# Optimization experiments

Hardware: AMD Instinct MI355X
Metric: run time of the kernel (lower is better)

The kernel has to match this reference:

```python
import jax, jax.numpy as jnp
import numpy as np

N = 131072        # total nodes
D = 256           # d_model (params.emb_dim)
STEPS = 16        # depth steps
G = N // STEPS    # nodes per depth step (equal-sized groups)
B = 16            # batch (number of trees); all lengths equal N//B
V = 1024          # len(id2word)
# op schedule: -1 leaf embedding, -2 numeric encoder, 0/1 unary ('sin','cos'), 2/3 binary ('add','mul')
SCHEDULE = [-1, -2, 0, 2, 1, 3, 0, 2, 1, 3, 0, 2, 1, 3, 0, 2]


def setup_inputs() -> dict:
    key = jax.random.key(0)
    ks = jax.random.split(key, 8)
    tokens = jax.random.randint(ks[0], (N,), 0, V, dtype=jnp.int32)
    # children of a node at depth d must already be computed: indices < d*G
    rng = np.random.default_rng(0)
    li = np.zeros(N, np.int32)
    ri = np.zeros(N, np.int32)
    for d in range(2, STEPS):
        li[d * G:(d + 1) * G] = rng.integers(0, d * G, G)
        ri[d * G:(d + 1) * G] = rng.integers(0, d * G, G)
    depths = jnp.repeat(jnp.arange(STEPS, dtype=jnp.int32), G)
    operation_order = jnp.array(SCHEDULE, dtype=jnp.int32)
    lengths = jnp.full((B,), N // B, dtype=jnp.int32)
    s = 0.05
    leaf_table = jax.random.normal(ks[1], (V, D), jnp.float32)
    num_W1 = jax.random.normal(ks[2], (D, 1), jnp.float32) * s
    num_b1 = jnp.zeros((D,), jnp.float32)
    num_W2 = jax.random.normal(ks[3], (D, D), jnp.float32) * s
    num_b2 = jnp.zeros((D,), jnp.float32)
    una_W = jax.random.normal(ks[4], (2, 4, D, D), jnp.float32) * s
    una_b = jnp.zeros((2, 4, D), jnp.float32)
    bin_W = jax.random.normal(ks[5], (2, 10, D, D), jnp.float32) * s
    bin_b = jnp.zeros((2, 5, D), jnp.float32)
    return dict(tokens=tokens, left_idx=jnp.asarray(li), right_idx=jnp.asarray(ri),
                depths=depths, operation_order=operation_order, lengths=lengths,
                leaf_table=leaf_table, num_W1=num_W1, num_b1=num_b1,
                num_W2=num_W2, num_b2=num_b2,
                una_W=una_W, una_b=una_b, bin_W=bin_W, bin_b=bin_b)


def _unary_cell(hc, W, b):
    # hc: [G, 2, D]; W: [4, D, D] (data, forget, output, input); b: [4, D]
    h, c = hc[:, 0], hc[:, 1]
    g = jnp.einsum('nd,ked->kne', h, W) + b[:, None, :]  # y = h @ W_k.T + b_k
    i = jax.nn.sigmoid(g[0])
    f = jax.nn.sigmoid(g[1])
    o = jax.nn.sigmoid(g[2])
    u = jnp.tanh(g[3])
    c2 = i * u + f * c
    h2 = o * jnp.tanh(c2)
    h2 = h2 / jnp.linalg.norm(h2)  # global (Frobenius) norm, as in torch h.norm(p=2)
    c2 = c2 / jnp.linalg.norm(c2)
    return jnp.stack([h2, c2], axis=1)


def _binary_cell(hcl, hcr, W, b):
    # W: [10, D, D] = (data_l, data_r, f_ll, f_lr, f_rl, f_rr, out_l, out_r, in_l, in_r)
    # b: [5, D] = (data, forget_l, forget_r, output, input)
    hl, cl = hcl[:, 0], hcl[:, 1]
    hr, cr = hcr[:, 0], hcr[:, 1]
    gl = jnp.einsum('nd,ked->kne', hl, W[jnp.array([0, 2, 4, 6, 8])])
    gr = jnp.einsum('nd,ked->kne', hr, W[jnp.array([1, 3, 5, 7, 9])])
    g = gl + gr + b[:, None, :]
    i = jax.nn.sigmoid(g[0])
    f_l = jax.nn.sigmoid(g[1])
    f_r = jax.nn.sigmoid(g[2])
    o = jax.nn.sigmoid(g[3])
    u = jnp.tanh(g[4])
    c2 = i * u + f_l * cl + f_r * cr
    h2 = o * jnp.tanh(c2)
    h2 = h2 / jnp.linalg.norm(h2)
    c2 = c2 / jnp.linalg.norm(c2)
    return jnp.stack([h2, c2], axis=1)


def reference(tokens, left_idx, right_idx, depths, operation_order, lengths,
              leaf_table, num_W1, num_b1, num_W2, num_b2,
              una_W, una_b, bin_W, bin_b):
    sched = np.asarray(operation_order).tolist()  # static dispatch schedule
    n = tokens.shape[0]
    steps = len(sched)
    g = n // steps
    d_model = leaf_table.shape[1]
    acts = jnp.zeros((n, 2, d_model), leaf_table.dtype)
    for d, op in enumerate(sched):
        s = d * g
        if op == -1:  # leaf embedding with max_norm=1.0 renorm (non-differentiable scale)
            e = leaf_table[tokens[s:s + g]]
            nrm = jnp.linalg.norm(e, axis=-1, keepdims=True)
            scale = jax.lax.stop_gradient(jnp.minimum(1.0, 1.0 / (nrm + 1e-7)))
            e = e * scale
            step_act = jnp.stack([e, jnp.zeros_like(e)], axis=1)
        elif op == -2:  # numeric encoder
            x = tokens[s:s + g].astype(leaf_table.dtype)[:, None]
            h1 = jax.nn.sigmoid(x @ num_W1.T + num_b1)
            e = jax.nn.sigmoid(h1 @ num_W2.T + num_b2)
            step_act = jnp.stack([e, jnp.zeros_like(e)], axis=1)
        elif op in (0, 1):  # unary LSTM cell: gather child then cell
            child = acts[left_idx[s:s + g]]
            step_act = _unary_cell(child, una_W[op], una_b[op])
        else:  # binary LSTM cell: gather both children
            l = acts[left_idx[s:s + g]]
            r = acts[right_idx[s:s + g]]
            step_act = _binary_cell(l, r, bin_W[op - 2], bin_b[op - 2])
        acts = jax.lax.dynamic_update_slice(acts, step_act, (s, 0, 0))
    hidden = acts[:, 0, :]  # [N, D]
    batch = lengths.shape[0]
    # all lengths equal -> pad_sequence is a reshape: [B, L, D]
    return hidden.reshape(batch, n // batch, d_model)
```

## Files before the change

### kernel.cpp

```cpp
#include <hip/hip_runtime.h>
#include <hip/hip_bf16.h>
#include <cstdint>

typedef unsigned short u16;
typedef unsigned int u32;
typedef __attribute__((ext_vector_type(4))) float floatx4;
typedef __attribute__((ext_vector_type(8))) short shortx8;

#define G_STEP 8192
#define N_TOTAL 131072
#define RHALF (1280*256)

__device__ __forceinline__ float bfu2f(u16 x){ return __uint_as_float(((unsigned)x)<<16); }
__device__ __forceinline__ u16 f2bfu(float x){ __hip_bfloat16 b = __float2bfloat16(x); return *reinterpret_cast<u16*>(&b); }
__device__ __forceinline__ float sigm(float x){ return 1.0f/(1.0f+__expf(-x)); }
__device__ __forceinline__ float tanh_(float x){
  float cx = fminf(fmaxf(x,-15.f),15.f);
  float e = __expf(2.f*cx);
  return (e-1.f)/(e+1.f);
}
__device__ __forceinline__ float invs(float x){ return 1.0f/sqrtf(x); }

__device__ __forceinline__ void gl16(const void* g, void* l){
  __builtin_amdgcn_global_load_lds((const __attribute__((address_space(1))) u32*)g,
                                   (__attribute__((address_space(3))) u32*)l, 16, 0, 0);
}

template<int V> __device__ __forceinline__ void wait_vml();
template<> __device__ __forceinline__ void wait_vml<0>(){ asm volatile("s_waitcnt vmcnt(0) lgkmcnt(0)" ::: "memory"); }
template<> __device__ __forceinline__ void wait_vml<6>(){ asm volatile("s_waitcnt vmcnt(6) lgkmcnt(0)" ::: "memory"); }
template<> __device__ __forceinline__ void wait_vml<7>(){ asm volatile("s_waitcnt vmcnt(7) lgkmcnt(0)" ::: "memory"); }

__device__ __forceinline__ void cvt8(const float* __restrict__ src, u16* __restrict__ dst){
  float4 a = *reinterpret_cast<const float4*>(src);
  float4 b = *reinterpret_cast<const float4*>(src+4);
  ushort4 o0; o0.x=f2bfu(a.x); o0.y=f2bfu(a.y); o0.z=f2bfu(a.z); o0.w=f2bfu(a.w);
  ushort4 o1; o1.x=f2bfu(b.x); o1.y=f2bfu(b.y); o1.z=f2bfu(b.z); o1.w=f2bfu(b.w);
  *reinterpret_cast<ushort4*>(dst)   = o0;
  *reinterpret_cast<ushort4*>(dst+4) = o1;
}

__global__ __launch_bounds__(256) void setup_kernel(
    const int* __restrict__ tokens, const float* __restrict__ leaf_table,
    const float* __restrict__ W1, const float* __restrict__ b1,
    const float* __restrict__ una_W, const float* __restrict__ bin_W,
    const float* __restrict__ num_W2,
    u16* __restrict__ wbu, u16* __restrict__ wbb, u16* __restrict__ wbn,
    u16* __restrict__ h1, u16* __restrict__ H, u16* __restrict__ C,
    float* __restrict__ sumsq)
{
  const int b = blockIdx.x, tid = threadIdx.x;
  if (b < 256){
    int row = b*8 + (tid>>5), d0 = (tid&31)*8;
    int op = row>>10, w = row&1023;
    int gate = (w>>4)&3, e = ((w>>6)<<4) | (w&15);
    cvt8(una_W + (size_t)((op*4+gate)*256 + e)*256 + d0, wbu + (size_t)row*256 + d0);
  } else if (b < 896){
    int row = (b-256)*8 + (tid>>5), d0 = (tid&31)*8;
    int ob = row / 2560, rem = row - ob*2560;
    int lr = rem / 1280, rw = rem - lr*1280;
    int eblk = rw / 80, rem2 = rw - eblk*80;
    int gate = rem2 >> 4, el = rem2 & 15;
    int e = eblk*16 + el;
    cvt8(bin_W + (size_t)((ob*10 + 2*gate + lr)*256 + e)*256 + d0, wbb + (size_t)row*256 + d0);
  } else if (b < 928){
    int row = (b-896)*8 + (tid>>5), d0 = (tid&31)*8;
    cvt8(num_W2 + (size_t)row*256 + d0, wbn + (size_t)row*256 + d0);
  } else if (b < 2976){
    int wave = tid >> 6, lane = tid & 63;
    int node = (b-928)*4 + wave;
    int t = tokens[node];
    const float4 e4 = *reinterpret_cast<const float4*>(leaf_table + (size_t)t*256 + lane*4);
    float ss = e4.x*e4.x + e4.y*e4.y + e4.z*e4.z + e4.w*e4.w;
    #pragma unroll
    for (int o = 32; o; o >>= 1) ss += __shfl_down(ss, o);
    ss = __shfl(ss, 0);
    float scale = fminf(1.0f, 1.0f/(sqrtf(ss) + 1e-7f));
    ushort4 hv;
    hv.x = f2bfu(e4.x*scale); hv.y = f2bfu(e4.y*scale);
    hv.z = f2bfu(e4.z*scale); hv.w = f2bfu(e4.w*scale);
    ushort4 zv; zv.x = zv.y = zv.z = zv.w = 0;
    *reinterpret_cast<ushort4*>(H + (size_t)node*256 + lane*4) = hv;
    *reinterpret_cast<ushort4*>(C + (size_t)node*256 + lane*4) = zv;
  } else if (b < 4000){
    int flat = (b-2976)*2048 + tid*8;
    int n = flat >> 8, d0 = flat & 255;
    float x = (float)tokens[G_STEP + n];
    float4 w0 = *reinterpret_cast<const float4*>(W1 + d0);
    float4 w1 = *reinterpret_cast<const float4*>(W1 + d0 + 4);
    float4 c0 = *reinterpret_cast<const float4*>(b1 + d0);
    float4 c1 = *reinterpret_cast<const float4*>(b1 + d0 + 4);
    ushort4 o0, o1;
    o0.x = f2bfu(sigm(x*w0.x + c0.x)); o0.y = f2bfu(sigm(x*w0.y + c0.y));
    o0.z = f2bfu(sigm(x*w0.z + c0.z)); o0.w = f2bfu(sigm(x*w0.w + c0.w));
    o1.x = f2bfu(sigm(x*w1.x + c1.x)); o1.y = f2bfu(sigm(x*w1.y + c1.y));
    o1.z = f2bfu(sigm(x*w1.z + c1.z)); o1.w = f2bfu(sigm(x*w1.w + c1.w));
    *reinterpret_cast<ushort4*>(h1 + flat)     = o0;
    *reinterpret_cast<ushort4*>(h1 + flat + 4) = o1;
  } else {
    if (tid < 32) sumsq[tid] = ((tid & 15) < 2) ? 1.0f : 0.0f;
  }
}

template<int MODE>
__global__ __launch_bounds__(512, 2) void gemm_fused(
    const u16* __restrict__ Asrc, const int* __restrict__ lidx,
    const int* __restrict__ ridx, const u16* __restrict__ Wb,
    const float* __restrict__ bias, const u16* __restrict__ Cin,
    float* __restrict__ sumsq, u16* __restrict__ H, u16* __restrict__ C,
    int sbase, int step)
{
  constexpr int NG  = (MODE==0) ? 1 : (MODE==1 ? 4 : 5);
  constexpr int NBR = (MODE==2) ? 160 : 128;
  constexpr int NT  = (MODE==2) ? 8 : 4;
  constexpr int WN  = (MODE==2) ? 80 : 64;
  constexpr int NFR = WN/16;
  constexpr int NBG = NBR/8;

  __shared__ u16 SA[3][256][64];
  __shared__ u16 SB[3][NBR][64];
  __shared__ float scH[16];
  __shared__ float scC[16];
  __shared__ float red[16];

  const int tid  = threadIdx.x;
  const int lane = tid & 63, wave = tid >> 6;

  const int bid = blockIdx.x;
  const int jj  = bid >> 3;
  const int bx  = (bid & 7) + 8*(jj & 3);
  const int by  = jj >> 2;
  const int mbase = bx*256;
  const int nbase = by*NBR;

  const int l15 = lane & 15, kg = lane >> 4;
  const int wm = (wave >> 1)*64, wn = (wave & 1)*WN;

  if (MODE != 0){
    if (tid < 16)      scH[tid]    = invs(sumsq[tid]);
    else if (tid < 32) scC[tid-16] = invs(sumsq[tid]);
  }

  const int rhi = lane >> 3;
  const int lc  = (lane & 7) ^ rhi;

  const u16* aL[4]; const u16* aR[4];
  #pragma unroll
  for (int g = 0; g < 4; g++){
    int r = (wave*4 + g)*8 + rhi;
    int gr;
    if constexpr (MODE==0) gr = mbase + r;
    else                   gr = lidx[sbase + mbase + r];
    aL[g] = Asrc + (size_t)gr*256 + lc*8;
    if constexpr (MODE==2)
      aR[g] = Asrc + (size_t)ridx[sbase + mbase + r]*256 + lc*8;
  }
  const int nbg_w = (MODE==2) ? ((wave < 4) ? 3 : 2) : 2;
  const int bg0   = (MODE==2) ? ((wave < 4) ? wave*3 : 12 + (wave-4)*2) : wave*2;
  const u16* bP[3];
  #pragma unroll
  for (int g = 0; g < 3; g++){
    int gg = bg0 + g;
    if (gg >= NBG) gg = NBG-1;
    bP[g] = Wb + (size_t)(nbase + gg*8 + rhi)*256 + lc*8;
  }

  floatx4 accL[4][NFR];
  #pragma unroll
  for (int i = 0; i < 4; i++)
    #pragma unroll
    for (int j2 = 0; j2 < NFR; j2++) accL[i][j2] = (floatx4)(0.0f);
  floatx4 accR[(MODE==2)?4:1][(MODE==2)?NFR:1];
  if constexpr (MODE==2){
    #pragma unroll
    for (int i = 0; i < 4; i++)
      #pragma unroll
      for (int j2 = 0; j2 < NFR; j2++) accR[i][j2] = (floatx4)(0.0f);
  }

  auto stage = [&](int t){
    const int slot = t % 3;
    const int kk = t*64;
    #pragma unroll
    for (int g = 0; g < 4; g++){
      const u16* ga;
      if constexpr (MODE==2){ ga = (kk >= 256) ? aR[g] + (kk-256) : aL[g] + kk; }
      else                  { ga = aL[g] + kk; }
      gl16(ga, &SA[slot][(wave*4 + g)*8][0]);
    }
    #pragma unroll
    for (int g = 0; g < 3; g++){
      if (g < nbg_w){
        const u16* gb;
        if constexpr (MODE==2){ gb = (kk >= 256) ? bP[g] + RHALF + (kk-256) : bP[g] + kk; }
        else                  { gb = bP[g] + kk; }
        gl16(gb, &SB[slot][(bg0 + g)*8][0]);
      }
    }
  };

  stage(0);
  stage(1);
  if (MODE==2 && wave < 4) wait_vml<7>(); else wait_vml<6>();
  __builtin_amdgcn_s_barrier();

  #pragma unroll
  for (int t = 0; t < NT; t++){
    const int slot = t % 3;
    if (t + 2 < NT) stage(t+2);

    {
      shortx8 af[4], bfr[NFR];
      const int pc = (kg ^ (l15 & 7)) * 8;
      #pragma unroll
      for (int i = 0; i < 4; i++)
        af[i] = *reinterpret_cast<const shortx8*>(&SA[slot][wm + i*16 + l15][pc]);
      #pragma unroll
      for (int n = 0; n < NFR; n++)
        bfr[n] = *reinterpret_cast<const shortx8*>(&SB[slot][wn + n*16 + l15][pc]);
      if (MODE==2 && t >= 4){
        #pragma unroll
        for (int mi = 0; mi < 4; mi++)
          #pragma unroll
          for (int ni = 0; ni < NFR; ni++)
            accR[mi][ni] = __builtin_amdgcn_mfma_f32_16x16x32_bf16(af[mi], bfr[ni], accR[mi][ni], 0, 0, 0);
      } else {
        #pragma unroll
        for (int mi = 0; mi < 4; mi++)
          #pragma unroll
          for (int ni = 0; ni < NFR; ni++)
            accL[mi][ni] = __builtin_amdgcn_mfma_f32_16x16x32_bf16(af[mi], bfr[ni], accL[mi][ni], 0, 0, 0);
      }
    }
    {
      shortx8 af[4], bfr[NFR];
      const int pc = ((4 + kg) ^ (l15 & 7)) * 8;
      #pragma unroll
      for (int i = 0; i < 4; i++)
        af[i] = *reinterpret_cast<const shortx8*>(&SA[slot][wm + i*16 + l15][pc]);
      #pragma unroll
      for (int n = 0; n < NFR; n++)
        bfr[n] = *reinterpret_cast<const shortx8*>(&SB[slot][wn + n*16 + l15][pc]);
      if (MODE==2 && t >= 4){
        #pragma unroll
        for (int mi = 0; mi < 4; mi++)
          #pragma unroll
          for (int ni = 0; ni < NFR; ni++)
            accR[mi][ni] = __builtin_amdgcn_mfma_f32_16x16x32_bf16(af[mi], bfr[ni], accR[mi][ni], 0, 0, 0);
      } else {
        #pragma unroll
        for (int mi = 0; mi < 4; mi++)
          #pragma unroll
          for (int ni = 0; ni < NFR; ni++)
            accL[mi][ni] = __builtin_amdgcn_mfma_f32_16x16x32_bf16(af[mi], bfr[ni], accL[mi][ni], 0, 0, 0);
      }
    }

    if (t + 1 < NT){
      if (t + 2 < NT){
        if (MODE==2 && wave < 4) wait_vml<7>(); else wait_vml<6>();
      } else wait_vml<0>();
      __builtin_amdgcn_s_barrier();
    }
  }

  if constexpr (MODE == 0){
    float bb[4];
    #pragma unroll
    for (int ni = 0; ni < 4; ni++) bb[ni] = bias[nbase + wn + ni*16 + l15];
    #pragma unroll
    for (int mi = 0; mi < 4; mi++){
      #pragma unroll
      for (int r = 0; r < 4; r++){
        int node = sbase + mbase + wm + mi*16 + kg*4 + r;
        u16* hp = H + (size_t)node*256 + nbase + wn + l15;
        u16* cp = C + (size_t)node*256 + nbase + wn + l15;
        #pragma unroll
        for (int ni = 0; ni < 4; ni++){
          hp[ni*16] = f2bfu(sigm(accL[mi][ni][r] + bb[ni]));
          cp[ni*16] = 0;
        }
      }
    }
  } else {
    const int eb = by*2 + (wave & 1);
    const int e  = eb*16 + l15;
    float bb[NG];
    #pragma unroll
    for (int g = 0; g < NG; g++) bb[g] = bias[g*256 + e];
    float hss = 0.f, css = 0.f;
    #pragma unroll
    for (int mi = 0; mi < 4; mi++){
      #pragma unroll
      for (int r = 0; r < 4; r++){
        int orow = mbase + wm + mi*16 + kg*4 + r;
        int node = sbase + orow;
        int chl = lidx[node];
        float sl = scH[chl >> 13];
        float cl = bfu2f(Cin[(size_t)chl*256 + e]) * scC[chl >> 13];
        float c2, h2;
        if constexpr (MODE == 1){
          float i_ = sigm(accL[mi][0][r]*sl + bb[0]);
          float f_ = sigm(accL[mi][1][r]*sl + bb[1]);
          float o_ = sigm(accL[mi][2][r]*sl + bb[2]);
          float u_ = tanh_(accL[mi][3][r]*sl + bb[3]);
          c2 = i_*u_ + f_*cl;
          h2 = o_*tanh_(c2);
        } else {
          int chr = ridx[node];
          float sr = scH[chr >> 13];
          float cr = bfu2f(Cin[(size_t)chr*256 + e]) * scC[chr >> 13];
          float g0 = accL[mi][0][r]*sl + accR[mi][0][r]*sr + bb[0];
          float g1 = accL[mi][1][r]*sl + accR[mi][1][r]*sr + bb[1];
          float g2 = accL[mi][2][r]*sl + accR[mi][2][r]*sr + bb[2];
          float g3 = accL[mi][3][r]*sl + accR[mi][3][r]*sr + bb[3];
          float g4 = accL[mi][4][r]*sl + accR[mi][4][r]*sr + bb[4];
          float i_ = sigm(g0);
          float fl = sigm(g1);
          float fr = sigm(g2);
          float o_ = sigm(g3);
          float u_ = tanh_(g4);
          c2 = i_*u_ + fl*cl + fr*cr;
          h2 = o_*tanh_(c2);
        }
        H[(size_t)node*256 + e] = f2bfu(h2);
        C[(size_t)node*256 + e] = f2bfu(c2);
        hss += h2*h2;
        css += c2*c2;
      }
    }
    #pragma unroll
    for (int o = 32; o; o >>= 1){ hss += __shfl_down(hss, o); css += __shfl_down(css, o); }
    if (lane == 0){ red[wave] = hss; red[8+wave] = css; }
    __syncthreads();
    if (tid == 0){
      float s = 0.f;
      #pragma unroll
      for (int w = 0; w < 8; w++) s += red[w];
      atomicAdd(&sumsq[step], s);
    }
    if (tid == 64){
      float s = 0.f;
      #pragma unroll
      for (int w = 0; w < 8; w++) s += red[8+w];
      atomicAdd(&sumsq[16 + step], s);
    }
  }
}

__global__ __launch_bounds__(256) void out_kernel(
    const u16* __restrict__ H, const float* __restrict__ sumsq, float* __restrict__ out)
{
  size_t base = ((size_t)blockIdx.x*256 + threadIdx.x)*8;
  int n = (int)(base >> 8);
  float s = invs(sumsq[n >> 13]);
  const uint4 v = *reinterpret_cast<const uint4*>(H + base);
  float4 o0, o1;
  o0.x = bfu2f((u16)(v.x & 0xffff))*s; o0.y = bfu2f((u16)(v.x >> 16))*s;
  o0.z = bfu2f((u16)(v.y & 0xffff))*s; o0.w = bfu2f((u16)(v.y >> 16))*s;
  o1.x = bfu2f((u16)(v.z & 0xffff))*s; o1.y = bfu2f((u16)(v.z >> 16))*s;
  o1.z = bfu2f((u16)(v.w & 0xffff))*s; o1.w = bfu2f((u16)(v.w >> 16))*s;
  *reinterpret_cast<float4*>(out + base)     = o0;
  *reinterpret_cast<float4*>(out + base + 4) = o1;
}

extern "C" void kernel_launch(void* const* d_in, const int* in_sizes, int n_in,
                              void* d_out, int out_size, void* d_ws, size_t ws_size,
                              hipStream_t stream)
{
  const int*   tokens     = (const int*)d_in[0];
  const int*   lidx       = (const int*)d_in[1];
  const int*   ridx       = (const int*)d_in[2];
  const float* leaf_table = (const float*)d_in[6];
  const float* num_W1     = (const float*)d_in[7];
  const float* num_b1     = (const float*)d_in[8];
  const float* num_W2     = (const float*)d_in[9];
  const float* num_b2     = (const float*)d_in[10];
  const float* una_W      = (const float*)d_in[11];
  const float* una_b      = (const float*)d_in[12];
  const float* bin_W      = (const float*)d_in[13];
  const float* bin_b      = (const float*)d_in[14];

  char* ws = (char*)d_ws;
  size_t off = 0;
  u16* H   = (u16*)(ws + off); off += (size_t)N_TOTAL*256*2;
  u16* wbu = (u16*)(ws + off); off += (size_t)2048*256*2;
  u16* wbb = (u16*)(ws + off); off += (size_t)5120*256*2;
  u16* wbn = (u16*)(ws + off); off += (size_t)256*256*2;
  u16* h1  = (u16*)(ws + off); off += (size_t)G_STEP*256*2;
  float* sumsq = (float*)(ws + off); off += 32*4;

  u16* C = (u16*)d_out;

  setup_kernel<<<4001, 256, 0, stream>>>(tokens, leaf_table, num_W1, num_b1,
                                         una_W, bin_W, num_W2,
                                         wbu, wbb, wbn, h1, H, C, sumsq);
  gemm_fused<0><<<64, 512, 0, stream>>>(
      h1, nullptr, nullptr, wbn, num_b2, nullptr, sumsq, H, C, G_STEP, 1);

  const int sched[16] = {-1,-2,0,2,1,3,0,2,1,3,0,2,1,3,0,2};
  for (int d = 2; d < 16; d++){
    int op = sched[d];
    int sbase = d*G_STEP;
    if (op == 0 || op == 1){
      gemm_fused<1><<<256, 512, 0, stream>>>(
          H, lidx, nullptr, wbu + (size_t)op*1024*256,
          una_b + (size_t)op*4*256, C, sumsq, H, C, sbase, d);
    } else {
      int o2 = op - 2;
      gemm_fused<2><<<256, 512, 0, stream>>>(
          H, lidx, ridx, wbb + (size_t)o2*2*1280*256,
          bin_b + (size_t)o2*5*256, C, sumsq, H, C, sbase, d);
    }
  }
  out_kernel<<<(N_TOTAL*256)/(256*8), 256, 0, stream>>>(H, sumsq, (float*)d_out);
}
```

Measured before the change: 362.5 us.

## Deepen GEMM prefetch, raise MFMA priority, preload child indices, drop LDS scale tables

The prologue now stages three K-tiles instead of two, with adjusted vmcnt waits so the global-to-LDS pipeline runs one tile deeper. MFMA blocks are wrapped in s_setprio to favour the matrix issue. Child indices are loaded into registers before the GEMM instead of in the epilogue, and the shared-memory norm-scale tables are replaced by direct reads of sumsq with an inverse sqrt in the epilogue. The C buffer moves from the output into workspace. This adds register pressure, and a computed kf ratio appears unused.

```diff
diff --git a/kernel.cpp b/kernel.cpp
--- a/kernel.cpp
+++ b/kernel.cpp
@@ -30,6 +30,8 @@
 template<> __device__ __forceinline__ void wait_vml<0>(){ asm volatile("s_waitcnt vmcnt(0) lgkmcnt(0)" ::: "memory"); }
 template<> __device__ __forceinline__ void wait_vml<6>(){ asm volatile("s_waitcnt vmcnt(6) lgkmcnt(0)" ::: "memory"); }
 template<> __device__ __forceinline__ void wait_vml<7>(){ asm volatile("s_waitcnt vmcnt(7) lgkmcnt(0)" ::: "memory"); }
+template<> __device__ __forceinline__ void wait_vml<12>(){ asm volatile("s_waitcnt vmcnt(12) lgkmcnt(0)" ::: "memory"); }
+template<> __device__ __forceinline__ void wait_vml<14>(){ asm volatile("s_waitcnt vmcnt(14) lgkmcnt(0)" ::: "memory"); }
 
 __device__ __forceinline__ void cvt8(const float* __restrict__ src, u16* __restrict__ dst){
   float4 a = *reinterpret_cast<const float4*>(src);
@@ -119,8 +121,6 @@
 
   __shared__ u16 SA[3][256][64];
   __shared__ u16 SB[3][NBR][64];
-  __shared__ float scH[16];
-  __shared__ float scC[16];
   __shared__ float red[16];
 
   const int tid  = threadIdx.x;
@@ -136,13 +136,25 @@
   const int l15 = lane & 15, kg = lane >> 4;
   const int wm = (wave >> 1)*64, wn = (wave & 1)*WN;
 
-  if (MODE != 0){
-    if (tid < 16)      scH[tid]    = invs(sumsq[tid]);
-    else if (tid < 32) scC[tid-16] = invs(sumsq[tid]);
-  }
-
   const int rhi = lane >> 3;
   const int lc  = (lane & 7) ^ rhi;
+
+  int chl_[4][4];
+  int chr_[(MODE==2)?4:1][(MODE==2)?4:1];
+  float kf[(MODE==2)?4:1][(MODE==2)?4:1];
+  if constexpr (MODE != 0){
+    #pragma unroll
+    for (int mi = 0; mi < 4; mi++)
+      #pragma unroll
+      for (int r = 0; r < 4; r++){
+        int node = sbase + mbase + wm + mi*16 + kg*4 + r;
+        chl_[mi][r] = lidx[node];
+        if constexpr (MODE==2){
+          chr_[mi][r] = ridx[node];
+          kf[mi][r] = sqrtf(sumsq[chr_[mi][r] >> 13] / sumsq[chl_[mi][r] >> 13]);
+        }
+      }
+  }
 
   const u16* aL[4]; const u16* aR[4];
   #pragma unroll
@@ -201,13 +213,14 @@
 
   stage(0);
   stage(1);
-  if (MODE==2 && wave < 4) wait_vml<7>(); else wait_vml<6>();
+  stage(2);
+  if (MODE==2 && wave < 4) wait_vml<14>(); else wait_vml<12>();
   __builtin_amdgcn_s_barrier();
 
   #pragma unroll
   for (int t = 0; t < NT; t++){
     const int slot = t % 3;
-    if (t + 2 < NT) stage(t+2);
+    if (t >= 1 && t + 2 < NT) stage(t+2);
 
     {
       shortx8 af[4], bfr[NFR];
@@ -218,6 +231,7 @@
       #pragma unroll
       for (int n = 0; n < NFR; n++)
         bfr[n] = *reinterpret_cast<const shortx8*>(&SB[slot][wn + n*16 + l15][pc]);
+      __builtin_amdgcn_s_setprio(1);
       if (MODE==2 && t >= 4){
         #pragma unroll
         for (int mi = 0; mi < 4; mi++)
@@ -231,6 +245,7 @@
           for (int ni = 0; ni < NFR; ni++)
             accL[mi][ni] = __builtin_amdgcn_mfma_f32_16x16x32_bf16(af[mi], bfr[ni], accL[mi][ni], 0, 0, 0);
       }
+      __builtin_amdgcn_s_setprio(0);
     }
     {
       shortx8 af[4], bfr[NFR];
@@ -241,6 +256,7 @@
       #pragma unroll
       for (int n = 0; n < NFR; n++)
         bfr[n] = *reinterpret_cast<const shortx8*>(&SB[slot][wn + n*16 + l15][pc]);
+      __builtin_amdgcn_s_setprio(1);
       if (MODE==2 && t >= 4){
         #pragma unroll
         for (int mi = 0; mi < 4; mi++)
@@ -254,6 +270,7 @@
           for (int ni = 0; ni < NFR; ni++)
             accL[mi][ni] = __builtin_amdgcn_mfma_f32_16x16x32_bf16(af[mi], bfr[ni], accL[mi][ni], 0, 0, 0);
       }
+      __builtin_amdgcn_s_setprio(0);
     }
 
     if (t + 1 < NT){
@@ -283,8 +300,7 @@
       }
     }
   } else {
-    const int eb = by*2 + (wave & 1);
-    const int e  = eb*16 + l15;
+    const int e = (by*2 + (wave & 1))*16 + l15;
     float bb[NG];
     #pragma unroll
     for (int g = 0; g < NG; g++) bb[g] = bias[g*256 + e];
@@ -293,11 +309,10 @@
     for (int mi = 0; mi < 4; mi++){
       #pragma unroll
       for (int r = 0; r < 4; r++){
-        int orow = mbase + wm + mi*16 + kg*4 + r;
-        int node = sbase + orow;
-        int chl = lidx[node];
-        float sl = scH[chl >> 13];
-        float cl = bfu2f(Cin[(size_t)chl*256 + e]) * scC[chl >> 13];
+        int node = sbase + mbase + wm + mi*16 + kg*4 + r;
+        int chl = chl_[mi][r];
+        float sl = invs(sumsq[chl >> 13]);
+        float cl = bfu2f(Cin[(size_t)chl*256 + e]) * invs(sumsq[16 + (chl >> 13)]);
         float c2, h2;
         if constexpr (MODE == 1){
           float i_ = sigm(accL[mi][0][r]*sl + bb[0]);
@@ -307,9 +322,9 @@
           c2 = i_*u_ + f_*cl;
           h2 = o_*tanh_(c2);
         } else {
-          int chr = ridx[node];
-          float sr = scH[chr >> 13];
-          float cr = bfu2f(Cin[(size_t)chr*256 + e]) * scC[chr >> 13];
+          int chr = chr_[mi][r];
+          float sr = invs(sumsq[chr >> 13]);
+          float cr = bfu2f(Cin[(size_t)chr*256 + e]) * invs(sumsq[16 + (chr >> 13)]);
           float g0 = accL[mi][0][r]*sl + accR[mi][0][r]*sr + bb[0];
           float g1 = accL[mi][1][r]*sl + accR[mi][1][r]*sr + bb[1];
           float g2 = accL[mi][2][r]*sl + accR[mi][2][r]*sr + bb[2];
@@ -388,9 +403,8 @@
   u16* wbb = (u16*)(ws + off); off += (size_t)5120*256*2;
   u16* wbn = (u16*)(ws + off); off += (size_t)256*256*2;
   u16* h1  = (u16*)(ws + off); off += (size_t)G_STEP*256*2;
-  float* sumsq = (float*)(ws + off); off += 32*4;
-
-  u16* C = (u16*)d_out;
+  float* sumsq = (float*)(ws + off); off += 256;
+  u16* C   = (u16*)(ws + off); off += (size_t)N_TOTAL*256*2;
 
   setup_kernel<<<4001, 256, 0, stream>>>(tokens, leaf_table, num_W1, num_b1,
                                          una_W, bin_W, num_W2,
```

New measurement: 466.5 us. 1.29x slower.
